# Optimization experiments

Hardware: AMD Instinct MI355X
Metric: run time of the kernel (lower is better)

Reference implementation:

```python
import jax, jax.numpy as jnp
import numpy as np

H = 64  # hidden_size

def _lstm_layer(x_tbd, W_ih, W_hh, b_ih, b_hh):
    """x_tbd: [T, B, D] -> outputs [T, B, H]. PyTorch gate order i,f,g,o."""
    T, B, _ = x_tbd.shape
    # input contribution precomputed for all timesteps: [T, B, 4H]
    xg = jnp.einsum('tbd,gd->tbg', x_tbd, W_ih) + b_ih + b_hh

    def step(carry, xg_t):
        h, c = carry
        gates = xg_t + h @ W_hh.T  # [B, 4H]
        i, f, g, o = jnp.split(gates, 4, axis=-1)
        i = jax.nn.sigmoid(i)
        f = jax.nn.sigmoid(f)
        g = jnp.tanh(g)
        o = jax.nn.sigmoid(o)
        c = f * c + i * g
        h = o * jnp.tanh(c)
        return (h, c), h

    h0 = jnp.zeros((B, H), dtype=x_tbd.dtype)
    c0 = jnp.zeros((B, H), dtype=x_tbd.dtype)
    _, hs = jax.lax.scan(step, (h0, c0), xg)
    return hs  # [T, B, H]


def setup_inputs() -> dict:
    key = jax.random.key(0)
    ks = jax.random.split(key, 16)
    B, T, D = 1024, 512, 32
    s = 1.0 / np.sqrt(H)  # PyTorch LSTM init scale
    return {
        'x': jax.random.normal(ks[0], (B, T, D), dtype=jnp.float32),
        'W_ih_l0': jax.random.uniform(ks[1], (4 * H, D), jnp.float32, -s, s),
        'W_hh_l0': jax.random.uniform(ks[2], (4 * H, H), jnp.float32, -s, s),
        'b_ih_l0': jax.random.uniform(ks[3], (4 * H,), jnp.float32, -s, s),
        'b_hh_l0': jax.random.uniform(ks[4], (4 * H,), jnp.float32, -s, s),
        'W_ih_l1': jax.random.uniform(ks[5], (4 * H, H), jnp.float32, -s, s),
        'W_hh_l1': jax.random.uniform(ks[6], (4 * H, H), jnp.float32, -s, s),
        'b_ih_l1': jax.random.uniform(ks[7], (4 * H,), jnp.float32, -s, s),
        'b_hh_l1': jax.random.uniform(ks[8], (4 * H,), jnp.float32, -s, s),
        'fc1_w': jax.random.uniform(ks[9], (H // 2, H), jnp.float32, -s, s),
        'fc1_b': jax.random.uniform(ks[10], (H // 2,), jnp.float32, -s, s),
        'fc2_w': jax.random.uniform(ks[11], (1, H // 2), jnp.float32, -0.25, 0.25),
        'fc2_b': jax.random.uniform(ks[12], (1,), jnp.float32, -0.25, 0.25),
    }


def reference(x, W_ih_l0, W_hh_l0, b_ih_l0, b_hh_l0,
              W_ih_l1, W_hh_l1, b_ih_l1, b_hh_l1,
              fc1_w, fc1_b, fc2_w, fc2_b):
    x_tbd = jnp.transpose(x, (1, 0, 2))  # [T, B, D]
    h1 = _lstm_layer(x_tbd, W_ih_l0, W_hh_l0, b_ih_l0, b_hh_l0)   # [T, B, H]
    h2 = _lstm_layer(h1,   W_ih_l1, W_hh_l1, b_ih_l1, b_hh_l1)   # [T, B, H]
    last = h2[-1]                       # [B, H] == lstm_out[:, -1, :]
    out = jax.nn.relu(last @ fc1_w.T + fc1_b)  # dropout is identity at eval
    out = out @ fc2_w.T + fc2_b         # [B, 1]
    return out
```

## Files before the change

kernel.cpp:

```cpp
#include <hip/hip_runtime.h>
#include <math.h>
#include <stdint.h>


namespace {

constexpr int Hh = 64, Dd = 32, Tt = 512;
constexpr float LOG2E = 1.4426950408889634f;

typedef _Float16 f16x8 __attribute__((ext_vector_type(8)));
typedef float f32x4 __attribute__((ext_vector_type(4)));

__device__ __forceinline__ f32x4 mfma(f16x8 a, f16x8 b, f32x4 c) {
    return __builtin_amdgcn_mfma_f32_16x16x32_f16(a, b, c, 0, 0, 0);
}
__device__ __forceinline__ float rcpf(float x) { return __builtin_amdgcn_rcpf(x); }
__device__ __forceinline__ float exp2f_(float x) { return __builtin_amdgcn_exp2f(x); }
__device__ __forceinline__ float sigm_s(float p) { return rcpf(1.0f + exp2f_(-p)); }
__device__ __forceinline__ float tanh_s(float p) {
    return 1.0f - 2.0f * rcpf(exp2f_(p) + 1.0f);
}
__device__ __forceinline__ float tanh_n(float c) {
    return 1.0f - 2.0f * rcpf(exp2f_(c * (2.0f * LOG2E)) + 1.0f);
}
__device__ __forceinline__ f16x8 cvt8s(const float* p, float sc) {
    f16x8 r;
#pragma unroll
    for (int e = 0; e < 8; ++e) r[e] = (_Float16)(p[e] * sc);
    return r;
}
__device__ __forceinline__ void bar_lgkm() {
    asm volatile("s_waitcnt lgkmcnt(0)\n\ts_barrier" ::: "memory");
}

__global__ __launch_bounds__(512, 2) void lstm_f16(
    const float* __restrict__ x,
    const float* __restrict__ Wih0,
    const float* __restrict__ Whh0,
    const float* __restrict__ bih0, const float* __restrict__ bhh0,
    const float* __restrict__ Wih1,
    const float* __restrict__ Whh1,
    const float* __restrict__ bih1, const float* __restrict__ bhh1,
    const float* __restrict__ fc1w,
    const float* __restrict__ fc1b,
    const float* __restrict__ fc2w,
    const float* __restrict__ fc2b,
    float* __restrict__ out)
{
    __shared__ __align__(16) _Float16 s_h0[2][2][16][8];
    __shared__ __align__(16) _Float16 s_h1[2][2][16][8];
    __shared__ float s_hf[Hh][5];
    __shared__ float s_fcw[32 * 65];
    __shared__ float s_fc[32][5];

    const int tid = threadIdx.x;
    const int w = tid >> 6;
    const int l = tid & 63;
    const int ar = l & 15;
    const int akb = l >> 4;
    const int cq = l >> 4;
    const int cj = l & 15;
    const int cb = cj & 3;
    const int dd = cj >> 2;
    const bool isL1w = (w >= 4);
    const int wl = w & 3;
    const int b0 = blockIdx.x * 4;

    const int r4 = ar & 3;
    const float sc = (r4 == 2) ? 2.0f * LOG2E : LOG2E;
    const int grow = r4 * 64 + 16 * wl + 4 * (ar >> 2);
    f16x8 Afr[4][4];
    if (!isL1w) {
#pragma unroll
        for (int i = 0; i < 4; ++i) {
            const int g = grow + i;
            Afr[i][0] = cvt8s(Wih0 + g * Dd + akb * 8, sc);
            Afr[i][1] = cvt8s(Whh0 + g * Hh + akb * 8, sc);
            Afr[i][2] = cvt8s(Whh0 + g * Hh + 32 + akb * 8, sc);
            Afr[i][3] = Afr[i][1];
        }
    } else {
#pragma unroll
        for (int i = 0; i < 4; ++i) {
            const int g = grow + i;
            Afr[i][0] = cvt8s(Wih1 + g * Hh + akb * 8, sc);
            Afr[i][1] = cvt8s(Wih1 + g * Hh + 32 + akb * 8, sc);
            Afr[i][2] = cvt8s(Whh1 + g * Hh + akb * 8, sc);
            Afr[i][3] = cvt8s(Whh1 + g * Hh + 32 + akb * 8, sc);
        }
    }

    const float* bi = isL1w ? bih1 : bih0;
    const float* bhp = isL1w ? bhh1 : bhh0;
    f32x4 biasT[4];
#pragma unroll
    for (int i = 0; i < 4; ++i)
#pragma unroll
        for (int r = 0; r < 4; ++r) {
            const float s2 = (r == 2) ? 2.0f * LOG2E : LOG2E;
            const int uu = 16 * wl + 4 * cq + i;
            biasT[i][r] = s2 * (bi[r * 64 + uu] + bhp[r * 64 + uu]);
        }

    const int ub = 16 * wl + 4 * cq + dd;
    const int kf_h = ub >> 5;
    const int row_h = ((ub & 31) >> 3) * 4 + cb;
    const int e_h = ub & 7;
    _Float16* const wsel = isL1w ? &s_h1[1][kf_h][row_h][e_h]
                                 : &s_h0[0][kf_h][row_h][e_h];
    const int wdelta = isL1w ? -256 : 256;

    const int rrow = (l >> 4) * 4 + (l & 3);

    const float* xbase = x + ((size_t)(b0 + cb) * Tt) * Dd + akb * 8;

    if (tid < 256) ((int*)s_h0)[tid] = 0;
    else           ((int*)s_h1)[tid - 256] = 0;

    float4 xr0, xr1;
    f16x8 xcur;
    if (!isL1w) {
        xr0 = *(const float4*)(xbase);
        xr1 = *(const float4*)(xbase + 4);
#pragma unroll
        for (int e = 0; e < 4; ++e) {
            xcur[e] = (_Float16)xr0[e];
            xcur[4 + e] = (_Float16)xr1[e];
        }
        xr0 = *(const float4*)(xbase + Dd);
        xr1 = *(const float4*)(xbase + Dd + 4);
    }
    float cst = 0.f;
    __syncthreads();

#pragma unroll 2
    for (int t = 0; t < Tt; ++t) {
        const int pr = t & 1;
        const f16x8 b0a = *(const f16x8*)&s_h0[pr ^ 1][0][rrow][0];
        const f16x8 b0b = *(const f16x8*)&s_h0[pr ^ 1][1][rrow][0];

        f32x4 acc[4];
        if (!isL1w) {
#pragma unroll
            for (int i = 0; i < 4; ++i) {
                f32x4 a = mfma(Afr[i][0], xcur, biasT[i]);
                a = mfma(Afr[i][1], b0a, a);
                a = mfma(Afr[i][2], b0b, a);
                acc[i] = a;
            }
            f16x8 xn;
#pragma unroll
            for (int e = 0; e < 4; ++e) {
                xn[e] = (_Float16)xr0[e];
                xn[4 + e] = (_Float16)xr1[e];
            }
            const int tf = (t + 2 < Tt) ? (t + 2) : (Tt - 1);
            xr0 = *(const float4*)(xbase + (size_t)tf * Dd);
            xr1 = *(const float4*)(xbase + (size_t)tf * Dd + 4);
            xcur = xn;
        } else {
            const f16x8 b1a = *(const f16x8*)&s_h1[pr][0][rrow][0];
            const f16x8 b1b = *(const f16x8*)&s_h1[pr][1][rrow][0];
#pragma unroll
            for (int i = 0; i < 4; ++i) {
                f32x4 a = mfma(Afr[i][0], b0a, biasT[i]);
                a = mfma(Afr[i][1], b0b, a);
                a = mfma(Afr[i][2], b1a, a);
                a = mfma(Afr[i][3], b1b, a);
                acc[i] = a;
            }
        }

        const f32x4 g01 = (dd & 1) ? acc[1] : acc[0];
        const f32x4 g23 = (dd & 1) ? acc[3] : acc[2];
        const f32x4 gg = (dd & 2) ? g23 : g01;

        const float gi = sigm_s(gg[0]);
        const float gf = sigm_s(gg[1]);
        const float zz = tanh_s(gg[2]);
        const float go = sigm_s(gg[3]);
        float cn = gf * cst + gi * zz;
        float hv = go * tanh_n(cn);
        if (t == 0) {
            cn = isL1w ? 0.f : cn;
            hv = isL1w ? 0.f : hv;
        }
        cst = cn;
        *(wsel + (pr ? wdelta : 0)) = (_Float16)hv;
        bar_lgkm();
    }

    if (isL1w) {
        const f16x8 b0a = *(const f16x8*)&s_h0[1][0][rrow][0];
        const f16x8 b0b = *(const f16x8*)&s_h0[1][1][rrow][0];
        const f16x8 b1a = *(const f16x8*)&s_h1[0][0][rrow][0];
        const f16x8 b1b = *(const f16x8*)&s_h1[0][1][rrow][0];
        f32x4 acc[4];
#pragma unroll
        for (int i = 0; i < 4; ++i) {
            f32x4 a = mfma(Afr[i][0], b0a, biasT[i]);
            a = mfma(Afr[i][1], b0b, a);
            a = mfma(Afr[i][2], b1a, a);
            a = mfma(Afr[i][3], b1b, a);
            acc[i] = a;
        }
        const f32x4 g01 = (dd & 1) ? acc[1] : acc[0];
        const f32x4 g23 = (dd & 1) ? acc[3] : acc[2];
        const f32x4 gg = (dd & 2) ? g23 : g01;
        const float gi = sigm_s(gg[0]);
        const float gf = sigm_s(gg[1]);
        const float zz = tanh_s(gg[2]);
        const float go = sigm_s(gg[3]);
        const float cn = gf * cst + gi * zz;
        s_hf[ub][cb] = go * tanh_n(cn);
    }
    __syncthreads();

    for (int i2 = tid; i2 < 32 * 64; i2 += 512) {
        const int m = i2 >> 6, uu = i2 & 63;
        s_fcw[m * 65 + uu] = fc1w[i2];
    }
    __syncthreads();
    if (tid < 128) {
        const int m = tid >> 2, jj = tid & 3;
        float acc = fc1b[m];
#pragma unroll
        for (int uu = 0; uu < Hh; ++uu)
            acc = fmaf(s_fcw[m * 65 + uu], s_hf[uu][jj], acc);
        s_fc[m][jj] = fmaxf(acc, 0.f);
    }
    __syncthreads();
    if (tid < 4) {
        float acc = fc2b[0];
#pragma unroll
        for (int m = 0; m < 32; ++m)
            acc = fmaf(fc2w[m], s_fc[m][tid], acc);
        out[b0 + tid] = acc;
    }
}

}

extern "C" void kernel_launch(void* const* d_in, const int* in_sizes, int n_in,
                              void* d_out, int out_size, void* d_ws, size_t ws_size,
                              hipStream_t stream) {
    const float* x    = (const float*)d_in[0];
    const float* Wih0 = (const float*)d_in[1];
    const float* Whh0 = (const float*)d_in[2];
    const float* bih0 = (const float*)d_in[3];
    const float* bhh0 = (const float*)d_in[4];
    const float* Wih1 = (const float*)d_in[5];
    const float* Whh1 = (const float*)d_in[6];
    const float* bih1 = (const float*)d_in[7];
    const float* bhh1 = (const float*)d_in[8];
    const float* fc1w = (const float*)d_in[9];
    const float* fc1b = (const float*)d_in[10];
    const float* fc2w = (const float*)d_in[11];
    const float* fc2b = (const float*)d_in[12];
    float* out = (float*)d_out;

    lstm_f16<<<dim3(256), dim3(512), 0, stream>>>(
        x, Wih0, Whh0, bih0, bhh0, Wih1, Whh1, bih1, bhh1,
        fc1w, fc1b, fc2w, fc2b, out);
}
```

Baseline: 274.7 us.

## Replace per-step block barrier with ring buffer and LDS counter flags

Each timestep previously ended in a block-wide barrier over all eight waves. Now layer-0 and layer-1 waves talk through a DEP-deep ring of hidden-state slots with workgroup-scope acquire/release counters. Layer 0 can run ahead of layer 1 by several steps, and waves spin-wait only on the slots they need. The aim is to decouple the two layers' recurrences and remove lockstep barrier stalls. The cost is spin-polling with s_sleep and the risk of subtle memory-ordering bugs.

Result: no change. 271.7 us, median of 2 (-1.1%).

```diff
diff --git a/kernel.cpp b/kernel.cpp
--- a/kernel.cpp
+++ b/kernel.cpp
@@ -5,7 +5,7 @@
 
 namespace {
 
-constexpr int Hh = 64, Dd = 32, Tt = 512;
+constexpr int Hh = 64, Dd = 32, Tt = 512, DEP = 6;
 constexpr float LOG2E = 1.4426950408889634f;
 
 typedef _Float16 f16x8 __attribute__((ext_vector_type(8)));
@@ -29,8 +29,11 @@
     for (int e = 0; e < 8; ++e) r[e] = (_Float16)(p[e] * sc);
     return r;
 }
-__device__ __forceinline__ void bar_lgkm() {
-    asm volatile("s_waitcnt lgkmcnt(0)\n\ts_barrier" ::: "memory");
+__device__ __forceinline__ int ld_acq(const int* p) {
+    return __hip_atomic_load(p, __ATOMIC_ACQUIRE, __HIP_MEMORY_SCOPE_WORKGROUP);
+}
+__device__ __forceinline__ void add_rel(int* p, int v) {
+    __hip_atomic_fetch_add(p, v, __ATOMIC_RELEASE, __HIP_MEMORY_SCOPE_WORKGROUP);
 }
 
 __global__ __launch_bounds__(512, 2) void lstm_f16(
@@ -47,8 +50,11 @@
     const float* __restrict__ fc2b,
     float* __restrict__ out)
 {
-    __shared__ __align__(16) _Float16 s_h0[2][2][16][8];
-    __shared__ __align__(16) _Float16 s_h1[2][2][16][8];
+    __shared__ __align__(16) _Float16 s_h0[DEP][2][16][8];
+    __shared__ __align__(16) _Float16 s_h1[DEP][2][16][8];
+    __shared__ int s_cnt0[DEP];
+    __shared__ int s_cnt1[DEP];
+    __shared__ int s_cons;
     __shared__ float s_hf[Hh][5];
     __shared__ float s_fcw[32 * 65];
     __shared__ float s_fc[32][5];
@@ -106,22 +112,32 @@
     const int kf_h = ub >> 5;
     const int row_h = ((ub & 31) >> 3) * 4 + cb;
     const int e_h = ub & 7;
-    _Float16* const wsel = isL1w ? &s_h1[1][kf_h][row_h][e_h]
-                                 : &s_h0[0][kf_h][row_h][e_h];
-    const int wdelta = isL1w ? -256 : 256;
+    _Float16* const wb0 = &s_h0[0][kf_h][row_h][e_h];
+    _Float16* const wb1 = &s_h1[0][kf_h][row_h][e_h];
 
     const int rrow = (l >> 4) * 4 + (l & 3);
-
-    const float* xbase = x + ((size_t)(b0 + cb) * Tt) * Dd + akb * 8;
-
-    if (tid < 256) ((int*)s_h0)[tid] = 0;
-    else           ((int*)s_h1)[tid - 256] = 0;
-
-    float4 xr0, xr1;
-    f16x8 xcur;
+    const _Float16* const rb0 = &s_h0[0][0][rrow][0];
+    const _Float16* const rb1 = &s_h1[0][0][rrow][0];
+
+    {
+        int* p0 = (int*)s_h0;
+        int* p1 = (int*)s_h1;
+        for (int i = tid; i < DEP * 128; i += 512) { p0[i] = 0; p1[i] = 0; }
+        if (tid < DEP) {
+            s_cnt0[tid] = (tid == 0) ? 4 : 0;
+            s_cnt1[tid] = (tid == 0) ? 4 : 0;
+        }
+        if (tid == DEP) s_cons = 0;
+    }
+    __syncthreads();
+
+    float lasth = 0.f;
+
     if (!isL1w) {
-        xr0 = *(const float4*)(xbase);
-        xr1 = *(const float4*)(xbase + 4);
+        const float* xbase = x + ((size_t)(b0 + cb) * Tt) * Dd + akb * 8;
+        float4 xr0 = *(const float4*)(xbase);
+        float4 xr1 = *(const float4*)(xbase + 4);
+        f16x8 xcur;
 #pragma unroll
         for (int e = 0; e < 4; ++e) {
             xcur[e] = (_Float16)xr0[e];
@@ -129,18 +145,15 @@
         }
         xr0 = *(const float4*)(xbase + Dd);
         xr1 = *(const float4*)(xbase + Dd + 4);
-    }
-    float cst = 0.f;
-    __syncthreads();
-
-#pragma unroll 2
-    for (int t = 0; t < Tt; ++t) {
-        const int pr = t & 1;
-        const f16x8 b0a = *(const f16x8*)&s_h0[pr ^ 1][0][rrow][0];
-        const f16x8 b0b = *(const f16x8*)&s_h0[pr ^ 1][1][rrow][0];
-
-        f32x4 acc[4];
-        if (!isL1w) {
+
+        float cst = 0.f;
+        int rs = 0, tgt = 4;
+        for (int t = 0; t < Tt; ++t) {
+            while (ld_acq(&s_cnt0[rs]) < tgt) __builtin_amdgcn_s_sleep(1);
+            const f16x8 b0a = *(const f16x8*)(rb0 + rs * 256);
+            const f16x8 b0b = *(const f16x8*)(rb0 + rs * 256 + 128);
+
+            f32x4 acc[4];
 #pragma unroll
             for (int i = 0; i < 4; ++i) {
                 f32x4 a = mfma(Afr[i][0], xcur, biasT[i]);
@@ -158,9 +171,38 @@
             xr0 = *(const float4*)(xbase + (size_t)tf * Dd);
             xr1 = *(const float4*)(xbase + (size_t)tf * Dd + 4);
             xcur = xn;
-        } else {
-            const f16x8 b1a = *(const f16x8*)&s_h1[pr][0][rrow][0];
-            const f16x8 b1b = *(const f16x8*)&s_h1[pr][1][rrow][0];
+
+            const f32x4 g01 = (dd & 1) ? acc[1] : acc[0];
+            const f32x4 g23 = (dd & 1) ? acc[3] : acc[2];
+            const f32x4 gg = (dd & 2) ? g23 : g01;
+            const float gi = sigm_s(gg[0]);
+            const float gf = sigm_s(gg[1]);
+            const float zz = tanh_s(gg[2]);
+            const float go = sigm_s(gg[3]);
+            cst = gf * cst + gi * zz;
+            const float hv = go * tanh_n(cst);
+
+            const int ws = (rs + 1 == DEP) ? 0 : rs + 1;
+            if (t >= DEP - 1)
+                while (ld_acq(&s_cons) < 4 * (t - 4)) __builtin_amdgcn_s_sleep(1);
+            wb0[ws * 256] = (_Float16)hv;
+            if (l == 0) add_rel(&s_cnt0[ws], 1);
+            rs = ws;
+            if (rs == 0) tgt += 4;
+        }
+    } else {
+        float cst = 0.f;
+        int rs0 = 1, t0 = 4;
+        int rs1 = 0, t1 = 4;
+        for (int s = 0; s < Tt; ++s) {
+            while (ld_acq(&s_cnt0[rs0]) < t0) __builtin_amdgcn_s_sleep(1);
+            while (ld_acq(&s_cnt1[rs1]) < t1) __builtin_amdgcn_s_sleep(1);
+            const f16x8 b0a = *(const f16x8*)(rb0 + rs0 * 256);
+            const f16x8 b0b = *(const f16x8*)(rb0 + rs0 * 256 + 128);
+            const f16x8 b1a = *(const f16x8*)(rb1 + rs1 * 256);
+            const f16x8 b1b = *(const f16x8*)(rb1 + rs1 * 256 + 128);
+
+            f32x4 acc[4];
 #pragma unroll
             for (int i = 0; i < 4; ++i) {
                 f32x4 a = mfma(Afr[i][0], b0a, biasT[i]);
@@ -169,50 +211,28 @@
                 a = mfma(Afr[i][3], b1b, a);
                 acc[i] = a;
             }
-        }
-
-        const f32x4 g01 = (dd & 1) ? acc[1] : acc[0];
-        const f32x4 g23 = (dd & 1) ? acc[3] : acc[2];
-        const f32x4 gg = (dd & 2) ? g23 : g01;
-
-        const float gi = sigm_s(gg[0]);
-        const float gf = sigm_s(gg[1]);
-        const float zz = tanh_s(gg[2]);
-        const float go = sigm_s(gg[3]);
-        float cn = gf * cst + gi * zz;
-        float hv = go * tanh_n(cn);
-        if (t == 0) {
-            cn = isL1w ? 0.f : cn;
-            hv = isL1w ? 0.f : hv;
-        }
-        cst = cn;
-        *(wsel + (pr ? wdelta : 0)) = (_Float16)hv;
-        bar_lgkm();
-    }
-
-    if (isL1w) {
-        const f16x8 b0a = *(const f16x8*)&s_h0[1][0][rrow][0];
-        const f16x8 b0b = *(const f16x8*)&s_h0[1][1][rrow][0];
-        const f16x8 b1a = *(const f16x8*)&s_h1[0][0][rrow][0];
-        const f16x8 b1b = *(const f16x8*)&s_h1[0][1][rrow][0];
-        f32x4 acc[4];
-#pragma unroll
-        for (int i = 0; i < 4; ++i) {
-            f32x4 a = mfma(Afr[i][0], b0a, biasT[i]);
-            a = mfma(Afr[i][1], b0b, a);
-            a = mfma(Afr[i][2], b1a, a);
-            a = mfma(Afr[i][3], b1b, a);
-            acc[i] = a;
-        }
-        const f32x4 g01 = (dd & 1) ? acc[1] : acc[0];
-        const f32x4 g23 = (dd & 1) ? acc[3] : acc[2];
-        const f32x4 gg = (dd & 2) ? g23 : g01;
-        const float gi = sigm_s(gg[0]);
-        const float gf = sigm_s(gg[1]);
-        const float zz = tanh_s(gg[2]);
-        const float go = sigm_s(gg[3]);
-        const float cn = gf * cst + gi * zz;
-        s_hf[ub][cb] = go * tanh_n(cn);
+            const f32x4 g01 = (dd & 1) ? acc[1] : acc[0];
+            const f32x4 g23 = (dd & 1) ? acc[3] : acc[2];
+            const f32x4 gg = (dd & 2) ? g23 : g01;
+            const float gi = sigm_s(gg[0]);
+            const float gf = sigm_s(gg[1]);
+            const float zz = tanh_s(gg[2]);
+            const float go = sigm_s(gg[3]);
+            cst = gf * cst + gi * zz;
+            const float hv = go * tanh_n(cst);
+            lasth = hv;
+
+            wb1[rs0 * 256] = (_Float16)hv;
+            if (l == 0) {
+                add_rel(&s_cnt1[rs0], 1);
+                add_rel(&s_cons, 1);
+            }
+            rs1 = rs0;
+            t1 = t0;
+            rs0 = (rs0 + 1 == DEP) ? 0 : rs0 + 1;
+            if (rs0 == 0) t0 += 4;
+        }
+        s_hf[ub][cb] = lasth;
     }
     __syncthreads();
 
```

## Halve wavefronts per block, each wave computing two hidden-unit groups

Applied to the files above, without the earlier changes.

The block shrinks from 512 to 256 threads (2 waves per layer instead of 4), and each wave computes 8 gate tiles covering two 16-unit groups, keeping two cell states per lane. Fewer waves take part in each per-timestep barrier, which should make the barrier cheaper and give more independent MFMA work between barriers. The cost is twice the serial MFMA and activation work per wave on the critical path each step, and higher register pressure from doubled weight fragments.

Result: slower. 358.4 us (+30.5%).

```diff
diff --git a/kernel.cpp b/kernel.cpp
--- a/kernel.cpp
+++ b/kernel.cpp
@@ -33,7 +33,7 @@
     asm volatile("s_waitcnt lgkmcnt(0)\n\ts_barrier" ::: "memory");
 }
 
-__global__ __launch_bounds__(512, 2) void lstm_f16(
+__global__ __launch_bounds__(256, 1) void lstm_f16(
     const float* __restrict__ x,
     const float* __restrict__ Wih0,
     const float* __restrict__ Whh0,
@@ -61,28 +61,27 @@
     const int cq = l >> 4;
     const int cj = l & 15;
     const int cb = cj & 3;
-    const int dd = cj >> 2;
-    const bool isL1w = (w >= 4);
-    const int wl = w & 3;
+    const int dsel = cj >> 2;
+    const bool isL1w = (w >= 2);
+    const int wl = w & 1;
     const int b0 = blockIdx.x * 4;
 
     const int r4 = ar & 3;
     const float sc = (r4 == 2) ? 2.0f * LOG2E : LOG2E;
-    const int grow = r4 * 64 + 16 * wl + 4 * (ar >> 2);
-    f16x8 Afr[4][4];
+    const int gbase = r4 * 64 + 32 * wl + 4 * (ar >> 2);
+    f16x8 Afr[8][4];
     if (!isL1w) {
 #pragma unroll
-        for (int i = 0; i < 4; ++i) {
-            const int g = grow + i;
+        for (int i = 0; i < 8; ++i) {
+            const int g = gbase + (i & 3) + 16 * (i >> 2);
             Afr[i][0] = cvt8s(Wih0 + g * Dd + akb * 8, sc);
             Afr[i][1] = cvt8s(Whh0 + g * Hh + akb * 8, sc);
             Afr[i][2] = cvt8s(Whh0 + g * Hh + 32 + akb * 8, sc);
-            Afr[i][3] = Afr[i][1];
         }
     } else {
 #pragma unroll
-        for (int i = 0; i < 4; ++i) {
-            const int g = grow + i;
+        for (int i = 0; i < 8; ++i) {
+            const int g = gbase + (i & 3) + 16 * (i >> 2);
             Afr[i][0] = cvt8s(Wih1 + g * Hh + akb * 8, sc);
             Afr[i][1] = cvt8s(Wih1 + g * Hh + 32 + akb * 8, sc);
             Afr[i][2] = cvt8s(Whh1 + g * Hh + akb * 8, sc);
@@ -92,20 +91,20 @@
 
     const float* bi = isL1w ? bih1 : bih0;
     const float* bhp = isL1w ? bhh1 : bhh0;
-    f32x4 biasT[4];
-#pragma unroll
-    for (int i = 0; i < 4; ++i)
+    f32x4 biasT[8];
+#pragma unroll
+    for (int i = 0; i < 8; ++i)
 #pragma unroll
         for (int r = 0; r < 4; ++r) {
             const float s2 = (r == 2) ? 2.0f * LOG2E : LOG2E;
-            const int uu = 16 * wl + 4 * cq + i;
+            const int uu = 32 * wl + 4 * cq + (i & 3) + 16 * (i >> 2);
             biasT[i][r] = s2 * (bi[r * 64 + uu] + bhp[r * 64 + uu]);
         }
 
-    const int ub = 16 * wl + 4 * cq + dd;
-    const int kf_h = ub >> 5;
-    const int row_h = ((ub & 31) >> 3) * 4 + cb;
-    const int e_h = ub & 7;
+    const int u1 = 32 * wl + 4 * cq + dsel;
+    const int kf_h = u1 >> 5;
+    const int row_h = ((u1 & 31) >> 3) * 4 + cb;
+    const int e_h = u1 & 7;
     _Float16* const wsel = isL1w ? &s_h1[1][kf_h][row_h][e_h]
                                  : &s_h0[0][kf_h][row_h][e_h];
     const int wdelta = isL1w ? -256 : 256;
@@ -114,8 +113,8 @@
 
     const float* xbase = x + ((size_t)(b0 + cb) * Tt) * Dd + akb * 8;
 
-    if (tid < 256) ((int*)s_h0)[tid] = 0;
-    else           ((int*)s_h1)[tid - 256] = 0;
+    ((int*)s_h0)[tid] = 0;
+    ((int*)s_h1)[tid] = 0;
 
     float4 xr0, xr1;
     f16x8 xcur;
@@ -130,23 +129,22 @@
         xr0 = *(const float4*)(xbase + Dd);
         xr1 = *(const float4*)(xbase + Dd + 4);
     }
-    float cst = 0.f;
+    float cst1 = 0.f, cst2 = 0.f;
     __syncthreads();
 
 #pragma unroll 2
     for (int t = 0; t < Tt; ++t) {
         const int pr = t & 1;
-        const f16x8 b0a = *(const f16x8*)&s_h0[pr ^ 1][0][rrow][0];
-        const f16x8 b0b = *(const f16x8*)&s_h0[pr ^ 1][1][rrow][0];
-
-        f32x4 acc[4];
+
+        f32x4 acc[8];
         if (!isL1w) {
-#pragma unroll
-            for (int i = 0; i < 4; ++i) {
+            const f16x8 b0a = *(const f16x8*)&s_h0[pr ^ 1][0][rrow][0];
+            const f16x8 b0b = *(const f16x8*)&s_h0[pr ^ 1][1][rrow][0];
+#pragma unroll
+            for (int i = 0; i < 8; ++i) {
                 f32x4 a = mfma(Afr[i][0], xcur, biasT[i]);
                 a = mfma(Afr[i][1], b0a, a);
-                a = mfma(Afr[i][2], b0b, a);
-                acc[i] = a;
+                acc[i] = mfma(Afr[i][2], b0b, a);
             }
             f16x8 xn;
 #pragma unroll
@@ -161,62 +159,92 @@
         } else {
             const f16x8 b1a = *(const f16x8*)&s_h1[pr][0][rrow][0];
             const f16x8 b1b = *(const f16x8*)&s_h1[pr][1][rrow][0];
-#pragma unroll
-            for (int i = 0; i < 4; ++i) {
+            const f16x8 b0a = *(const f16x8*)&s_h0[pr ^ 1][0][rrow][0];
+            const f16x8 b0b = *(const f16x8*)&s_h0[pr ^ 1][1][rrow][0];
+#pragma unroll
+            for (int i = 0; i < 8; ++i) {
                 f32x4 a = mfma(Afr[i][0], b0a, biasT[i]);
                 a = mfma(Afr[i][1], b0b, a);
                 a = mfma(Afr[i][2], b1a, a);
-                a = mfma(Afr[i][3], b1b, a);
-                acc[i] = a;
+                acc[i] = mfma(Afr[i][3], b1b, a);
             }
         }
 
-        const f32x4 g01 = (dd & 1) ? acc[1] : acc[0];
-        const f32x4 g23 = (dd & 1) ? acc[3] : acc[2];
-        const f32x4 gg = (dd & 2) ? g23 : g01;
-
-        const float gi = sigm_s(gg[0]);
-        const float gf = sigm_s(gg[1]);
-        const float zz = tanh_s(gg[2]);
-        const float go = sigm_s(gg[3]);
-        float cn = gf * cst + gi * zz;
-        float hv = go * tanh_n(cn);
-        if (t == 0) {
-            cn = isL1w ? 0.f : cn;
-            hv = isL1w ? 0.f : hv;
-        }
-        cst = cn;
-        *(wsel + (pr ? wdelta : 0)) = (_Float16)hv;
+        const f32x4 sA01 = (dsel & 1) ? acc[1] : acc[0];
+        const f32x4 sA23 = (dsel & 1) ? acc[3] : acc[2];
+        const f32x4 gA = (dsel & 2) ? sA23 : sA01;
+        const f32x4 sB01 = (dsel & 1) ? acc[5] : acc[4];
+        const f32x4 sB23 = (dsel & 1) ? acc[7] : acc[6];
+        const f32x4 gB = (dsel & 2) ? sB23 : sB01;
+
+        float hv1, hv2;
+        {
+            const float gi = sigm_s(gA[0]);
+            const float gf = sigm_s(gA[1]);
+            const float zz = tanh_s(gA[2]);
+            const float go = sigm_s(gA[3]);
+            float cn = gf * cst1 + gi * zz;
+            float hv = go * tanh_n(cn);
+            if (t == 0) { cn = isL1w ? 0.f : cn; hv = isL1w ? 0.f : hv; }
+            cst1 = cn;
+            hv1 = hv;
+        }
+        {
+            const float gi = sigm_s(gB[0]);
+            const float gf = sigm_s(gB[1]);
+            const float zz = tanh_s(gB[2]);
+            const float go = sigm_s(gB[3]);
+            float cn = gf * cst2 + gi * zz;
+            float hv = go * tanh_n(cn);
+            if (t == 0) { cn = isL1w ? 0.f : cn; hv = isL1w ? 0.f : hv; }
+            cst2 = cn;
+            hv2 = hv;
+        }
+        _Float16* wp = wsel + (pr ? wdelta : 0);
+        wp[0] = (_Float16)hv1;
+        wp[64] = (_Float16)hv2;
         bar_lgkm();
     }
 
     if (isL1w) {
+        const f16x8 b1a = *(const f16x8*)&s_h1[0][0][rrow][0];
+        const f16x8 b1b = *(const f16x8*)&s_h1[0][1][rrow][0];
         const f16x8 b0a = *(const f16x8*)&s_h0[1][0][rrow][0];
         const f16x8 b0b = *(const f16x8*)&s_h0[1][1][rrow][0];
-        const f16x8 b1a = *(const f16x8*)&s_h1[0][0][rrow][0];
-        const f16x8 b1b = *(const f16x8*)&s_h1[0][1][rrow][0];
-        f32x4 acc[4];
-#pragma unroll
-        for (int i = 0; i < 4; ++i) {
+        f32x4 acc[8];
+#pragma unroll
+        for (int i = 0; i < 8; ++i) {
             f32x4 a = mfma(Afr[i][0], b0a, biasT[i]);
             a = mfma(Afr[i][1], b0b, a);
             a = mfma(Afr[i][2], b1a, a);
-            a = mfma(Afr[i][3], b1b, a);
-            acc[i] = a;
-        }
-        const f32x4 g01 = (dd & 1) ? acc[1] : acc[0];
-        const f32x4 g23 = (dd & 1) ? acc[3] : acc[2];
-        const f32x4 gg = (dd & 2) ? g23 : g01;
-        const float gi = sigm_s(gg[0]);
-        const float gf = sigm_s(gg[1]);
-        const float zz = tanh_s(gg[2]);
-        const float go = sigm_s(gg[3]);
-        const float cn = gf * cst + gi * zz;
-        s_hf[ub][cb] = go * tanh_n(cn);
-    }
-    __syncthreads();
-
-    for (int i2 = tid; i2 < 32 * 64; i2 += 512) {
+            acc[i] = mfma(Afr[i][3], b1b, a);
+        }
+        const f32x4 sA01 = (dsel & 1) ? acc[1] : acc[0];
+        const f32x4 sA23 = (dsel & 1) ? acc[3] : acc[2];
+        const f32x4 gA = (dsel & 2) ? sA23 : sA01;
+        const f32x4 sB01 = (dsel & 1) ? acc[5] : acc[4];
+        const f32x4 sB23 = (dsel & 1) ? acc[7] : acc[6];
+        const f32x4 gB = (dsel & 2) ? sB23 : sB01;
+        {
+            const float gi = sigm_s(gA[0]);
+            const float gf = sigm_s(gA[1]);
+            const float zz = tanh_s(gA[2]);
+            const float go = sigm_s(gA[3]);
+            const float cn = gf * cst1 + gi * zz;
+            s_hf[u1][cb] = go * tanh_n(cn);
+        }
+        {
+            const float gi = sigm_s(gB[0]);
+            const float gf = sigm_s(gB[1]);
+            const float zz = tanh_s(gB[2]);
+            const float go = sigm_s(gB[3]);
+            const float cn = gf * cst2 + gi * zz;
+            s_hf[u1 + 16][cb] = go * tanh_n(cn);
+        }
+    }
+    __syncthreads();
+
+    for (int i2 = tid; i2 < 32 * 64; i2 += 256) {
         const int m = i2 >> 6, uu = i2 & 63;
         s_fcw[m * 65 + uu] = fc1w[i2];
     }
@@ -259,7 +287,7 @@
     const float* fc2b = (const float*)d_in[12];
     float* out = (float*)d_out;
 
-    lstm_f16<<<dim3(256), dim3(512), 0, stream>>>(
+    lstm_f16<<<dim3(256), dim3(256), 0, stream>>>(
         x, Wih0, Whh0, bih0, bhh0, Wih1, Whh1, bih1, bhh1,
         fc1w, fc1b, fc2w, fc2b, out);
 }
```
